# Performance work log

Measured on AMD Instinct MI355X. Metric: run time of the kernel, lower is better.

The kernel has to match this reference:

```python
import jax, jax.numpy as jnp
import numpy as np

R = 16
ALPHA = 16.0
SCALE = ALPHA / max(1, R)  # alpha / max(1, r)


def setup_inputs() -> dict:
    key = jax.random.key(0)
    k1, k2, k3, k4, k5 = jax.random.split(key, 5)
    B, S, D_IN, D_OUT = 4, 4096, 4096, 4096
    x = jax.random.normal(k1, (B, S, D_IN), dtype=jnp.float32)
    weight = jax.random.normal(k2, (D_OUT, D_IN), dtype=jnp.float32) * (1.0 / np.sqrt(D_IN))
    bias = jax.random.normal(k3, (D_OUT,), dtype=jnp.float32)
    lora_A = jax.random.normal(k4, (R, D_IN), dtype=jnp.float32) * (1.0 / np.sqrt(D_IN))
    lora_B = jax.random.normal(k5, (D_OUT, R), dtype=jnp.float32) * (1.0 / np.sqrt(R))
    return {"x": x, "weight": weight, "bias": bias, "lora_A": lora_A, "lora_B": lora_B}


def reference(x, weight, bias, lora_A, lora_B):
    # base = F.linear(x, weight, bias) = x @ W^T + b
    base = jnp.einsum('bsi,oi->bso', x, weight) + bias
    # lora = x @ (B @ A)^T = (x @ A^T) @ B^T  (chained low-rank, same math)
    xa = jnp.einsum('bsi,ri->bsr', x, lora_A)   # [B,S,r]
    lora = jnp.einsum('bsr,or->bso', xa, lora_B)  # [B,S,out]
    return base + SCALE * lora
```

## Files before the change

### kernel.cpp

```cpp
#include <hip/hip_runtime.h>
#include <hip/hip_bf16.h>
#include <stdint.h>

#define M_DIM 16384
#define N_DIM 4096
#define K_DIM 4096
#define LORA_SCALE 1.0f

typedef _Float16 half8 __attribute__((ext_vector_type(8)));
typedef float f32x4 __attribute__((ext_vector_type(4)));

__global__ __launch_bounds__(256) void cvt_x_kernel(const float* __restrict__ x,
                                                    _Float16* __restrict__ xb) {
    size_t base = ((size_t)blockIdx.x * 256 + (size_t)threadIdx.x) * 8;
    f32x4 a = *(const f32x4*)(x + base);
    f32x4 b = *(const f32x4*)(x + base + 4);
    half8 h;
    h[0] = (_Float16)a[0]; h[1] = (_Float16)a[1];
    h[2] = (_Float16)a[2]; h[3] = (_Float16)a[3];
    h[4] = (_Float16)b[0]; h[5] = (_Float16)b[1];
    h[6] = (_Float16)b[2]; h[7] = (_Float16)b[3];
    *(half8*)(xb + base) = h;
}

__global__ __launch_bounds__(256) void prep_w_kernel(const float* __restrict__ W,
                                                     const float* __restrict__ lA,
                                                     const float* __restrict__ lB,
                                                     _Float16* __restrict__ wp) {
    __shared__ float A_lds[16][256];
    __shared__ float B_lds[256];
    const int t = threadIdx.x;
    const int n0 = blockIdx.x * 16;

    B_lds[t] = lB[(size_t)n0 * 16 + t];

    for (int kc = 0; kc < 16; ++kc) {
        const int k = kc * 256 + t;
        __syncthreads();
#pragma unroll
        for (int r = 0; r < 16; ++r) A_lds[r][t] = lA[(size_t)r * K_DIM + k];
        __syncthreads();
#pragma unroll 4
        for (int row = 0; row < 16; ++row) {
            float acc = W[(size_t)(n0 + row) * K_DIM + k];
            float dot = 0.f;
#pragma unroll
            for (int r = 0; r < 16; ++r) dot += B_lds[row * 16 + r] * A_lds[r][t];
            acc += LORA_SCALE * dot;
            wp[(size_t)(n0 + row) * K_DIM + k] = (_Float16)acc;
        }
    }
}

__device__ inline void load_lds16(const void* g, void* l) {
    __builtin_amdgcn_global_load_lds(
        (const __attribute__((address_space(1))) unsigned int*)(uintptr_t)g,
        (__attribute__((address_space(3))) unsigned int*)(uintptr_t)l,
        16, 0, 0);
}

__global__ __launch_bounds__(256) void gemm_bt_kernel(const _Float16* __restrict__ A,
                                                      const _Float16* __restrict__ B,
                                                      const float* __restrict__ bias,
                                                      float* __restrict__ C) {
    __shared__ _Float16 As[128 * 32];
    __shared__ _Float16 Bs[128 * 32];

    const int tid  = threadIdx.x;
    const int lane = tid & 63;
    const int wave = tid >> 6;
    const int quad = lane >> 4;
    const int r16  = lane & 15;
    const int wm   = wave >> 1;
    const int wn   = wave & 1;

    const int m0 = blockIdx.y * 128;
    const int n0 = blockIdx.x * 128;

    const int c0 = tid;
    const int c1 = tid + 256;

    const _Float16* gA0 = A + (size_t)(m0 + (c0 >> 2)) * K_DIM + ((c0 & 3) << 3);
    const _Float16* gA1 = A + (size_t)(m0 + (c1 >> 2)) * K_DIM + ((c1 & 3) << 3);
    const _Float16* gB0 = B + (size_t)(n0 + (c0 >> 2)) * K_DIM + ((c0 & 3) << 3);
    const _Float16* gB1 = B + (size_t)(n0 + (c1 >> 2)) * K_DIM + ((c1 & 3) << 3);
    _Float16* lA0 = &As[c0 * 8];
    _Float16* lA1 = &As[c1 * 8];
    _Float16* lB0 = &Bs[c0 * 8];
    _Float16* lB1 = &Bs[c1 * 8];

    f32x4 acc[4][4] = {};

    for (int kt = 0; kt < K_DIM / 32; ++kt) {
        load_lds16(gA0, lA0);
        load_lds16(gA1, lA1);
        load_lds16(gB0, lB0);
        load_lds16(gB1, lB1);
        gA0 += 32; gA1 += 32; gB0 += 32; gB1 += 32;

        __syncthreads();

        half8 af[4], bf[4];
#pragma unroll
        for (int i = 0; i < 4; ++i)
            af[i] = *(const half8*)&As[(wm * 64 + i * 16 + r16) * 32 + quad * 8];
#pragma unroll
        for (int j = 0; j < 4; ++j)
            bf[j] = *(const half8*)&Bs[(wn * 64 + j * 16 + r16) * 32 + quad * 8];

#pragma unroll
        for (int i = 0; i < 4; ++i)
#pragma unroll
            for (int j = 0; j < 4; ++j)
                acc[i][j] = __builtin_amdgcn_mfma_f32_16x16x32_f16(af[i], bf[j],
                                                                   acc[i][j], 0, 0, 0);

        __syncthreads();
    }

#pragma unroll
    for (int j = 0; j < 4; ++j) {
        const int n = n0 + wn * 64 + j * 16 + r16;
        const float bv = bias[n];
#pragma unroll
        for (int i = 0; i < 4; ++i) {
            const int mbase = m0 + wm * 64 + i * 16 + quad * 4;
#pragma unroll
            for (int r = 0; r < 4; ++r) {
                C[(size_t)(mbase + r) * N_DIM + n] = acc[i][j][r] + bv;
            }
        }
    }
}

extern "C" void kernel_launch(void* const* d_in, const int* in_sizes, int n_in,
                              void* d_out, int out_size, void* d_ws, size_t ws_size,
                              hipStream_t stream) {
    const float* x      = (const float*)d_in[0];
    const float* weight = (const float*)d_in[1];
    const float* bias   = (const float*)d_in[2];
    const float* lora_A = (const float*)d_in[3];
    const float* lora_B = (const float*)d_in[4];
    float* out = (float*)d_out;

    _Float16* xb = (_Float16*)d_ws;
    _Float16* wp = (_Float16*)((char*)d_ws + (size_t)M_DIM * K_DIM * 2);

    cvt_x_kernel<<<dim3((M_DIM * (size_t)K_DIM) / (256 * 8)), dim3(256), 0, stream>>>(x, xb);
    prep_w_kernel<<<dim3(N_DIM / 16), dim3(256), 0, stream>>>(weight, lora_A, lora_B, wp);
    gemm_bt_kernel<<<dim3(N_DIM / 128, M_DIM / 128), dim3(256), 0, stream>>>(xb, wp, bias, out);
}
```

Before: 1.147 ms.

## Replace 128x128 GEMM with double-buffered 256x256 swizzled-LDS tile kernel

```diff
diff --git a/kernel.cpp b/kernel.cpp
--- a/kernel.cpp
+++ b/kernel.cpp
@@ -1,11 +1,15 @@
 #include <hip/hip_runtime.h>
-#include <hip/hip_bf16.h>
 #include <stdint.h>
 
 #define M_DIM 16384
 #define N_DIM 4096
 #define K_DIM 4096
 #define LORA_SCALE 1.0f
+
+#define BM 256
+#define BN 256
+#define BK 64
+#define NT (K_DIM / BK)
 
 typedef _Float16 half8 __attribute__((ext_vector_type(8)));
 typedef float f32x4 __attribute__((ext_vector_type(4)));
@@ -52,79 +56,146 @@
     }
 }
 
-__device__ inline void load_lds16(const void* g, void* l) {
+__device__ __forceinline__ void load_lds16(const void* g, void* l) {
     __builtin_amdgcn_global_load_lds(
         (const __attribute__((address_space(1))) unsigned int*)(uintptr_t)g,
         (__attribute__((address_space(3))) unsigned int*)(uintptr_t)l,
         16, 0, 0);
 }
 
-__global__ __launch_bounds__(256) void gemm_bt_kernel(const _Float16* __restrict__ A,
-                                                      const _Float16* __restrict__ B,
-                                                      const float* __restrict__ bias,
-                                                      float* __restrict__ C) {
-    __shared__ _Float16 As[128 * 32];
-    __shared__ _Float16 Bs[128 * 32];
+#define FENCE() do { \
+        asm volatile("s_waitcnt lgkmcnt(0)" ::: "memory"); \
+        __builtin_amdgcn_sched_barrier(0); \
+    } while (0)
+
+__global__ __launch_bounds__(512, 2) void gemm256_kernel(const _Float16* __restrict__ A,
+                                                         const _Float16* __restrict__ B,
+                                                         const float* __restrict__ bias,
+                                                         float* __restrict__ C) {
+    __shared__ _Float16 As[2][BM * BK];
+    __shared__ _Float16 Bs[2][BN * BK];
 
     const int tid  = threadIdx.x;
     const int lane = tid & 63;
     const int wave = tid >> 6;
+    const int wm   = wave >> 2;
+    const int wn   = wave & 3;
     const int quad = lane >> 4;
     const int r16  = lane & 15;
-    const int wm   = wave >> 1;
-    const int wn   = wave & 1;
-
-    const int m0 = blockIdx.y * 128;
-    const int n0 = blockIdx.x * 128;
-
-    const int c0 = tid;
-    const int c1 = tid + 256;
-
-    const _Float16* gA0 = A + (size_t)(m0 + (c0 >> 2)) * K_DIM + ((c0 & 3) << 3);
-    const _Float16* gA1 = A + (size_t)(m0 + (c1 >> 2)) * K_DIM + ((c1 & 3) << 3);
-    const _Float16* gB0 = B + (size_t)(n0 + (c0 >> 2)) * K_DIM + ((c0 & 3) << 3);
-    const _Float16* gB1 = B + (size_t)(n0 + (c1 >> 2)) * K_DIM + ((c1 & 3) << 3);
-    _Float16* lA0 = &As[c0 * 8];
-    _Float16* lA1 = &As[c1 * 8];
-    _Float16* lB0 = &Bs[c0 * 8];
-    _Float16* lB1 = &Bs[c1 * 8];
-
-    f32x4 acc[4][4] = {};
-
-    for (int kt = 0; kt < K_DIM / 32; ++kt) {
-        load_lds16(gA0, lA0);
-        load_lds16(gA1, lA1);
-        load_lds16(gB0, lB0);
-        load_lds16(gB1, lB1);
-        gA0 += 32; gA1 += 32; gB0 += 32; gB1 += 32;
-
-        __syncthreads();
-
-        half8 af[4], bf[4];
-#pragma unroll
-        for (int i = 0; i < 4; ++i)
-            af[i] = *(const half8*)&As[(wm * 64 + i * 16 + r16) * 32 + quad * 8];
-#pragma unroll
-        for (int j = 0; j < 4; ++j)
-            bf[j] = *(const half8*)&Bs[(wn * 64 + j * 16 + r16) * 32 + quad * 8];
-
-#pragma unroll
-        for (int i = 0; i < 4; ++i)
-#pragma unroll
-            for (int j = 0; j < 4; ++j)
-                acc[i][j] = __builtin_amdgcn_mfma_f32_16x16x32_f16(af[i], bf[j],
-                                                                   acc[i][j], 0, 0, 0);
-
-        __syncthreads();
-    }
+    const int swz  = r16 & 7;
+    const int cb   = (quad ^ swz) << 3;
+
+    const int bid = blockIdx.x;
+    const int id  = (bid & 7) * (1024 / 8) + (bid >> 3);
+    const int tm  = id >> 4;
+    const int tn  = id & 15;
+    const int m0  = tm * BM;
+    const int n0  = tn * BN;
+
+    const int u8 = tid & 7;
+    const _Float16* ga[4];
+    const _Float16* gb[4];
+    int lof[4];
+#pragma unroll
+    for (int l = 0; l < 4; ++l) {
+        const int c   = l * 512 + tid;
+        const int row = c >> 3;
+        const int sc  = (u8 ^ (row & 7)) << 3;
+        ga[l]  = A + (size_t)(m0 + row) * K_DIM + sc;
+        gb[l]  = B + (size_t)(n0 + row) * K_DIM + sc;
+        lof[l] = c << 3;
+    }
+
+    const int ab = (wm * 128 + r16) * BK;
+    const int bb = (wn * 64 + r16) * BK;
+
+    f32x4 acc[8][4] = {};
+
+#define STAGE(P) do { \
+        _Pragma("unroll") \
+        for (int l = 0; l < 4; ++l) { load_lds16(ga[l], &As[P][lof[l]]); ga[l] += BK; } \
+        _Pragma("unroll") \
+        for (int l = 0; l < 4; ++l) { load_lds16(gb[l], &Bs[P][lof[l]]); gb[l] += BK; } \
+    } while (0)
+
+#define MFMA_Q(ILO, JLO, BF) \
+        __builtin_amdgcn_s_setprio(1); \
+        _Pragma("unroll") \
+        for (int i = 0; i < 4; ++i) \
+            _Pragma("unroll") \
+            for (int j = 0; j < 2; ++j) { \
+                acc[(ILO) + i][(JLO) + j] = __builtin_amdgcn_mfma_f32_16x16x32_f16( \
+                    a[i][0], BF[j][0], acc[(ILO) + i][(JLO) + j], 0, 0, 0); \
+                acc[(ILO) + i][(JLO) + j] = __builtin_amdgcn_mfma_f32_16x16x32_f16( \
+                    a[i][1], BF[j][1], acc[(ILO) + i][(JLO) + j], 0, 0, 0); \
+            } \
+        __builtin_amdgcn_s_setprio(0);
+
+#define COMPUTE(P) do { \
+        half8 a[4][2], b0[2][2], b1[2][2]; \
+        _Pragma("unroll") \
+        for (int i = 0; i < 4; ++i) { \
+            a[i][0] = *(const half8*)&As[P][ab + (i * 16) * BK + cb]; \
+            a[i][1] = *(const half8*)&As[P][ab + (i * 16) * BK + (cb ^ 32)]; \
+        } \
+        _Pragma("unroll") \
+        for (int j = 0; j < 2; ++j) { \
+            b0[j][0] = *(const half8*)&Bs[P][bb + (j * 16) * BK + cb]; \
+            b0[j][1] = *(const half8*)&Bs[P][bb + (j * 16) * BK + (cb ^ 32)]; \
+        } \
+        MFMA_Q(0, 0, b0) \
+        _Pragma("unroll") \
+        for (int j = 0; j < 2; ++j) { \
+            b1[j][0] = *(const half8*)&Bs[P][bb + ((j + 2) * 16) * BK + cb]; \
+            b1[j][1] = *(const half8*)&Bs[P][bb + ((j + 2) * 16) * BK + (cb ^ 32)]; \
+        } \
+        MFMA_Q(0, 2, b1) \
+        _Pragma("unroll") \
+        for (int i = 0; i < 4; ++i) { \
+            a[i][0] = *(const half8*)&As[P][ab + ((i + 4) * 16) * BK + cb]; \
+            a[i][1] = *(const half8*)&As[P][ab + ((i + 4) * 16) * BK + (cb ^ 32)]; \
+        } \
+        MFMA_Q(4, 0, b0) \
+        MFMA_Q(4, 2, b1) \
+    } while (0)
+
+    STAGE(0);
+    STAGE(1);
+    asm volatile("s_waitcnt vmcnt(8)" ::: "memory");
+    __builtin_amdgcn_s_barrier();
+
+#pragma unroll 1
+    for (int it = 0; it < NT / 2 - 1; ++it) {
+        COMPUTE(0);
+        FENCE();
+        __builtin_amdgcn_s_barrier();
+        STAGE(0);
+        asm volatile("s_waitcnt vmcnt(8)" ::: "memory");
+        __builtin_amdgcn_s_barrier();
+        COMPUTE(1);
+        FENCE();
+        __builtin_amdgcn_s_barrier();
+        STAGE(1);
+        asm volatile("s_waitcnt vmcnt(8)" ::: "memory");
+        __builtin_amdgcn_s_barrier();
+    }
+    COMPUTE(0);
+    FENCE();
+    asm volatile("s_waitcnt vmcnt(0)" ::: "memory");
+    __builtin_amdgcn_s_barrier();
+    COMPUTE(1);
+
+#undef COMPUTE
+#undef MFMA_Q
+#undef STAGE
 
 #pragma unroll
     for (int j = 0; j < 4; ++j) {
         const int n = n0 + wn * 64 + j * 16 + r16;
         const float bv = bias[n];
 #pragma unroll
-        for (int i = 0; i < 4; ++i) {
-            const int mbase = m0 + wm * 64 + i * 16 + quad * 4;
+        for (int i = 0; i < 8; ++i) {
+            const int mbase = m0 + wm * 128 + i * 16 + quad * 4;
 #pragma unroll
             for (int r = 0; r < 4; ++r) {
                 C[(size_t)(mbase + r) * N_DIM + n] = acc[i][j][r] + bv;
@@ -148,5 +219,5 @@
 
     cvt_x_kernel<<<dim3((M_DIM * (size_t)K_DIM) / (256 * 8)), dim3(256), 0, stream>>>(x, xb);
     prep_w_kernel<<<dim3(N_DIM / 16), dim3(256), 0, stream>>>(weight, lora_A, lora_B, wp);
-    gemm_bt_kernel<<<dim3(N_DIM / 128, M_DIM / 128), dim3(256), 0, stream>>>(xb, wp, bias, out);
-}
+    gemm256_kernel<<<dim3((M_DIM / BM) * (N_DIM / BN)), dim3(512), 0, stream>>>(xb, wp, bias, out);
+}
```

Result: faster. 1.029 ms (-10.3%).
